# Optimization experiments

Measured on AMD Instinct MI355X. Metric: run time of the kernel, lower is better.

The kernel has to match this reference:

```python
import jax, jax.numpy as jnp
import numpy as np

H = 1024
N_HEADS = 8
HEAD_DIM = H // N_HEADS
META_DIM = 256
VOCAB = 32000
MIN_W, MAX_W = 0.1, 5.0
LN_EPS = 1e-5


def _ln(x, g, b):
    mu = jnp.mean(x, axis=-1, keepdims=True)
    var = jnp.var(x, axis=-1, keepdims=True)
    return (x - mu) * jax.lax.rsqrt(var + LN_EPS) * g + b


def setup_inputs() -> dict:
    key = jax.random.key(0)
    ks = jax.random.split(key, 16)
    B, S = 4, 2048
    s = 0.02
    return {
        "hidden_states": jax.random.normal(ks[0], (B, S, H), jnp.float32),
        "token_ids": jax.random.randint(ks[1], (B, S), 0, VOCAB, jnp.int32),
        "attention_mask": jnp.ones((B, S), jnp.bool_),
        "pos_embed": jax.random.normal(ks[2], (1, S, H), jnp.float32),
        # torch nn.MultiheadAttention params
        "in_proj_w": jax.random.normal(ks[3], (3 * H, H), jnp.float32) * s,
        "in_proj_b": jnp.zeros((3 * H,), jnp.float32),
        "out_w": jax.random.normal(ks[4], (H, H), jnp.float32) * s,
        "out_b": jnp.zeros((H,), jnp.float32),
        # meta_network params (torch Linear convention: y = x @ W.T + b)
        "w1": jax.random.normal(ks[5], (META_DIM, 2 * H), jnp.float32) * s,
        "b1": jnp.zeros((META_DIM,), jnp.float32),
        "g1": jnp.ones((META_DIM,), jnp.float32),
        "beta1": jnp.zeros((META_DIM,), jnp.float32),
        "w2": jax.random.normal(ks[6], (META_DIM // 2, META_DIM), jnp.float32) * s,
        "b2": jnp.zeros((META_DIM // 2,), jnp.float32),
        "g2": jnp.ones((META_DIM // 2,), jnp.float32),
        "beta2": jnp.zeros((META_DIM // 2,), jnp.float32),
        "w3": jax.random.normal(ks[7], (1, META_DIM // 2), jnp.float32) * s,
        "b3": jnp.zeros((1,), jnp.float32),
        # tensorized ImportanceMemory.get_importance: one scalar per vocab id
        "importance_table": jax.random.uniform(ks[8], (VOCAB,), jnp.float32) * 0.1,
    }


def reference(hidden_states, token_ids, attention_mask, pos_embed,
              in_proj_w, in_proj_b, out_w, out_b,
              w1, b1, g1, beta1, w2, b2, g2, beta2, w3, b3,
              importance_table):
    B, S, _ = hidden_states.shape
    x = hidden_states + pos_embed[:, :S, :]

    # MultiheadAttention (batch_first, eval mode -> no dropout)
    qkv = x @ in_proj_w.T + in_proj_b                      # [B,S,3H]
    q, k, v = jnp.split(qkv, 3, axis=-1)
    q = q.reshape(B, S, N_HEADS, HEAD_DIM)
    k = k.reshape(B, S, N_HEADS, HEAD_DIM)
    v = v.reshape(B, S, N_HEADS, HEAD_DIM)
    scores = jnp.einsum('bqhd,bkhd->bhqk', q, k) / jnp.sqrt(jnp.float32(HEAD_DIM))
    scores = jnp.where(attention_mask[:, None, None, :], scores, jnp.float32(-1e9))
    attn = jax.nn.softmax(scores, axis=-1)
    ctx = jnp.einsum('bhqk,bkhd->bqhd', attn, v).reshape(B, S, H)
    attended = ctx @ out_w.T + out_b

    combined = jnp.concatenate([x, attended], axis=-1)     # [B,S,2H]
    h = jax.nn.relu(_ln(combined @ w1.T + b1, g1, beta1))
    h = jax.nn.relu(_ln(h @ w2.T + b2, g2, beta2))
    base_weights = (h @ w3.T + b3).squeeze(-1)             # [B,S]

    # tensorized per-token importance lookup + clamp (manual_weights empty)
    importance = importance_table[token_ids]               # gather [B,S]
    weight = jnp.clip(base_weights * (1.0 + importance), MIN_W, MAX_W)
    return jnp.where(attention_mask, weight, 0.0)
```

## Files before the change

kernel.cpp:

```cpp
#include <hip/hip_runtime.h>
#include <hip/hip_bf16.h>
#include <math.h>

typedef __bf16 bf16;
typedef bf16 bf16x8 __attribute__((ext_vector_type(8)));
typedef bf16 bf16x4 __attribute__((ext_vector_type(4)));
typedef float f32x4 __attribute__((ext_vector_type(4)));

#define HDIM 1024
#define NHEADS 8
#define HD 128
#define MD1 256
#define MD2 128
#define LNEPS 1e-5f

__device__ __forceinline__ f32x4 mfma16(bf16x8 a, bf16x8 b, f32x4 c) {
  return __builtin_amdgcn_mfma_f32_16x16x32_bf16(a, b, c, 0, 0, 0);
}

__device__ __forceinline__ void gload_lds16(const bf16* g, bf16* l) {
  __builtin_amdgcn_global_load_lds(
      (const __attribute__((address_space(1))) void*)g,
      (__attribute__((address_space(3))) void*)l, 16, 0, 0);
}

__global__ void k_prep_all(
    const float* __restrict__ hs, const float* __restrict__ pos,
    bf16* __restrict__ xbf, int SH, int nprep,
    const float* __restrict__ s0, bf16* __restrict__ d0, int n0,
    const float* __restrict__ s1, bf16* __restrict__ d1, int n1,
    const float* __restrict__ s2, bf16* __restrict__ d2, int n2,
    const float* __restrict__ s3, bf16* __restrict__ d3, int n3) {
  int i = (blockIdx.x * blockDim.x + threadIdx.x) * 4;
  if (i < nprep) {
    float4 a = *(const float4*)(hs + i);
    float4 p = *(const float4*)(pos + (i % SH));
    bf16x4 o;
    o[0] = (bf16)(a.x + p.x); o[1] = (bf16)(a.y + p.y);
    o[2] = (bf16)(a.z + p.z); o[3] = (bf16)(a.w + p.w);
    *(bf16x4*)(xbf + i) = o;
    return;
  }
  int j = i - nprep;
  const float* s; bf16* d;
  if (j < n0)                { s = s0 + j; d = d0 + j; }
  else if (j < n0 + n1)      { s = s1 + (j - n0); d = d1 + (j - n0); }
  else if (j < n0 + n1 + n2) { s = s2 + (j - n0 - n1); d = d2 + (j - n0 - n1); }
  else                       { s = s3 + (j - n0 - n1 - n2); d = d3 + (j - n0 - n1 - n2); }
  float4 v = *(const float4*)s;
  bf16x4 o;
  o[0] = (bf16)v.x; o[1] = (bf16)v.y; o[2] = (bf16)v.z; o[3] = (bf16)v.w;
  *(bf16x4*)d = o;
}

template<bool OUT_BF>
__global__ __launch_bounds__(256) void k_gemm128(
    const bf16* __restrict__ A, const bf16* __restrict__ Bw,
    const float* __restrict__ bias, void* __restrict__ out,
    int N, int K) {
  __shared__ bf16 As[128 * 32];
  __shared__ bf16 Bs[128 * 32];
  const int tid = threadIdx.x;
  const int w = tid >> 6, lane = tid & 63;
  const int quad = lane >> 4, l16 = lane & 15;
  const int wm = w & 1, wn = w >> 1;
  const int tm = blockIdx.x * 128, tn = blockIdx.y * 128;

  const int r0 = tid >> 2;
  const int f0 = (r0 ^ (r0 >> 2)) & 3;
  const int f1 = ((r0 + 64) ^ ((r0 + 64) >> 2)) & 3;
  const int c0 = (((tid & 3) ^ f0) * 8);
  const int c1 = (((tid & 3) ^ f1) * 8);
  const bf16* a0 = A + (size_t)(tm + r0) * K + c0;
  const bf16* a1 = A + (size_t)(tm + r0 + 64) * K + c1;
  const bf16* b0 = Bw + (size_t)(tn + r0) * K + c0;
  const bf16* b1 = Bw + (size_t)(tn + r0 + 64) * K + c1;
  bf16* lA = As + (size_t)tid * 8;
  bf16* lB = Bs + (size_t)tid * 8;

  f32x4 acc[4][4] = {};
  for (int k0 = 0; k0 < K; k0 += 32) {
    gload_lds16(a0 + k0, lA);
    gload_lds16(a1 + k0, lA + 2048);
    gload_lds16(b0 + k0, lB);
    gload_lds16(b1 + k0, lB + 2048);
    __syncthreads();
    bf16x8 af[4], bfr[4];
#pragma unroll
    for (int mt = 0; mt < 4; ++mt) {
      const int r = wm * 64 + mt * 16 + l16;
      af[mt] = *(const bf16x8*)&As[r * 32 + ((quad ^ ((r ^ (r >> 2)) & 3)) << 3)];
    }
#pragma unroll
    for (int nt = 0; nt < 4; ++nt) {
      const int r = wn * 64 + nt * 16 + l16;
      bfr[nt] = *(const bf16x8*)&Bs[r * 32 + ((quad ^ ((r ^ (r >> 2)) & 3)) << 3)];
    }
#pragma unroll
    for (int mt = 0; mt < 4; ++mt)
#pragma unroll
      for (int nt = 0; nt < 4; ++nt)
        acc[mt][nt] = mfma16(af[mt], bfr[nt], acc[mt][nt]);
    __syncthreads();
  }

#pragma unroll
  for (int nt = 0; nt < 4; ++nt) {
    const int col = tn + wn * 64 + nt * 16 + l16;
    const float bv = bias ? bias[col] : 0.f;
#pragma unroll
    for (int mt = 0; mt < 4; ++mt) {
#pragma unroll
      for (int i = 0; i < 4; ++i) {
        const int row = tm + wm * 64 + mt * 16 + quad * 4 + i;
        const float v = acc[mt][nt][i] + bv;
        if (OUT_BF) ((bf16*)out)[(size_t)row * N + col] = (bf16)v;
        else        ((float*)out)[(size_t)row * N + col] = v;
      }
    }
  }
}

__global__ __launch_bounds__(256) void k_gemm_qkv(
    const bf16* __restrict__ A, const bf16* __restrict__ Bw,
    const float* __restrict__ bias, bf16* __restrict__ Qo,
    bf16* __restrict__ Ko, bf16* __restrict__ VTo, int S, int K) {
  __shared__ bf16 As[128 * 32];
  __shared__ bf16 Bs[128 * 32];
  const int tid = threadIdx.x;
  const int w = tid >> 6, lane = tid & 63;
  const int quad = lane >> 4, l16 = lane & 15;
  const int wm = w & 1, wn = w >> 1;
  const int tm = blockIdx.x * 128, tn = blockIdx.y * 128;

  const int r0 = tid >> 2;
  const int f0 = (r0 ^ (r0 >> 2)) & 3;
  const int f1 = ((r0 + 64) ^ ((r0 + 64) >> 2)) & 3;
  const int c0 = (((tid & 3) ^ f0) * 8);
  const int c1 = (((tid & 3) ^ f1) * 8);
  const bf16* a0 = A + (size_t)(tm + r0) * K + c0;
  const bf16* a1 = A + (size_t)(tm + r0 + 64) * K + c1;
  const bf16* b0 = Bw + (size_t)(tn + r0) * K + c0;
  const bf16* b1 = Bw + (size_t)(tn + r0 + 64) * K + c1;
  bf16* lA = As + (size_t)tid * 8;
  bf16* lB = Bs + (size_t)tid * 8;

  f32x4 acc[4][4] = {};
  for (int k0 = 0; k0 < K; k0 += 32) {
    gload_lds16(a0 + k0, lA);
    gload_lds16(a1 + k0, lA + 2048);
    gload_lds16(b0 + k0, lB);
    gload_lds16(b1 + k0, lB + 2048);
    __syncthreads();
    bf16x8 af[4], bfr[4];
#pragma unroll
    for (int mt = 0; mt < 4; ++mt) {
      const int r = wm * 64 + mt * 16 + l16;
      af[mt] = *(const bf16x8*)&As[r * 32 + ((quad ^ ((r ^ (r >> 2)) & 3)) << 3)];
    }
#pragma unroll
    for (int nt = 0; nt < 4; ++nt) {
      const int r = wn * 64 + nt * 16 + l16;
      bfr[nt] = *(const bf16x8*)&Bs[r * 32 + ((quad ^ ((r ^ (r >> 2)) & 3)) << 3)];
    }
#pragma unroll
    for (int mt = 0; mt < 4; ++mt)
#pragma unroll
      for (int nt = 0; nt < 4; ++nt)
        acc[mt][nt] = mfma16(af[mt], bfr[nt], acc[mt][nt]);
    __syncthreads();
  }

  const int region = tn >> 10;
  const int btile = tm / S, s0 = tm % S;
#pragma unroll
  for (int nt = 0; nt < 4; ++nt) {
    const int col = tn + wn * 64 + nt * 16 + l16;
    const float bv = bias[col];
#pragma unroll
    for (int mt = 0; mt < 4; ++mt) {
      if (region == 2) {
        const int d = col - 2048, hh = d >> 7, dd = d & 127;
        const int sb = s0 + wm * 64 + mt * 16 + quad * 4;
        bf16x4 o4;
#pragma unroll
        for (int i = 0; i < 4; ++i) o4[i] = (bf16)(acc[mt][nt][i] + bv);
        *(bf16x4*)&VTo[((size_t)(btile * NHEADS + hh) * HD + dd) * S + sb] = o4;
      } else {
        bf16* dst = (region == 0) ? Qo : Ko;
        const int cc = (region == 0) ? col : col - 1024;
#pragma unroll
        for (int i = 0; i < 4; ++i) {
          const int row = tm + wm * 64 + mt * 16 + quad * 4 + i;
          dst[(size_t)row * HDIM + cc] = (bf16)(acc[mt][nt][i] + bv);
        }
      }
    }
  }
}

__global__ __launch_bounds__(256) void k_flash(
    const bf16* __restrict__ Qg, const bf16* __restrict__ Kg,
    const bf16* __restrict__ VTg, const int* __restrict__ mask,
    bf16* __restrict__ ctx, int S) {
  __shared__ bf16 Ks[64][136];
  __shared__ bf16 Vt[128 * 64];
  __shared__ bf16 Ps[8 * 1024];
  __shared__ float biass[64];
  const int tid = threadIdx.x, w = tid >> 6, lane = tid & 63;
  const int quad = lane >> 4, l16 = lane & 15;
  const int bh = blockIdx.y, b = bh / NHEADS, h = bh % NHEADS;
  const int q0 = blockIdx.x * 128 + w * 32;
  const size_t bS = (size_t)b * S;
  const bf16* Qb = Qg + bS * HDIM + h * HD;
  const bf16* Kb = Kg + bS * HDIM + h * HD;
  const bf16* Vb = VTg + (size_t)bh * HD * S;
  const int* mrow = mask + bS;

  bf16x8 qf[2][4];
#pragma unroll
  for (int qt = 0; qt < 2; ++qt)
#pragma unroll
    for (int s = 0; s < 4; ++s)
      qf[qt][s] = *(const bf16x8*)(Qb + (size_t)(q0 + qt * 16 + l16) * HDIM + s * 32 + quad * 8);

  float lsum[2][4] = {};
  f32x4 o[2][8] = {};
  const float scale2 = 0.08838834764831845f * 1.4426950408889634f;

  const int nchunk = S / 64;
  bf16x8 kreg[4], vreg[4];
  int mreg = (tid < 64) ? mrow[tid] : 0;
#pragma unroll
  for (int it = 0; it < 4; ++it) {
    const int cid = tid + it * 256;
    kreg[it] = *(const bf16x8*)(Kb + (size_t)(cid >> 4) * HDIM + (cid & 15) * 8);
    vreg[it] = *(const bf16x8*)(Vb + (size_t)(cid >> 3) * S + (cid & 7) * 8);
  }

  for (int c0 = 0; c0 < nchunk; ++c0) {
    __syncthreads();
#pragma unroll
    for (int it = 0; it < 4; ++it) {
      const int cid = tid + it * 256;
      *(bf16x8*)&Ks[cid >> 4][(cid & 15) * 8] = kreg[it];
      const int vd = cid >> 3, vkb = cid & 7;
      *(bf16x8*)&Vt[vd * 64 + ((vkb ^ (vd & 7)) << 3)] = vreg[it];
    }
    if (tid < 64) biass[tid] = mreg ? 0.f : -1e9f;
    __syncthreads();
    const int key0n = ((c0 + 1 < nchunk) ? c0 + 1 : c0) * 64;
    if (tid < 64) mreg = mrow[key0n + tid];
#pragma unroll
    for (int it = 0; it < 4; ++it) {
      const int cid = tid + it * 256;
      kreg[it] = *(const bf16x8*)(Kb + (size_t)(key0n + (cid >> 4)) * HDIM + (cid & 15) * 8);
      vreg[it] = *(const bf16x8*)(Vb + (size_t)(cid >> 3) * S + key0n + (cid & 7) * 8);
    }
    f32x4 s4[2][4] = {};
#pragma unroll
    for (int g = 0; g < 4; ++g)
#pragma unroll
      for (int s = 0; s < 4; ++s) {
        bf16x8 kf = *(const bf16x8*)&Ks[g * 16 + l16][s * 32 + quad * 8];
        s4[0][g] = mfma16(qf[0][s], kf, s4[0][g]);
        s4[1][g] = mfma16(qf[1][s], kf, s4[1][g]);
      }
#pragma unroll
    for (int qt = 0; qt < 2; ++qt) {
      const int base = (w * 2 + qt) * 1024;
#pragma unroll
      for (int g = 0; g < 4; ++g) {
        const float bias = biass[g * 16 + l16];
        const int kb2 = 2 * g + (l16 >> 3), klo = l16 & 7;
#pragma unroll
        for (int i = 0; i < 4; ++i) {
          const float p = exp2f(fmaf(s4[qt][g][i], scale2, bias));
          lsum[qt][i] += p;
          const int r = quad * 4 + i, fr = (r ^ (r >> 3)) & 7;
          Ps[base + r * 64 + ((kb2 ^ fr) << 3) + klo] = (bf16)p;
        }
      }
    }
    const int fl = (l16 ^ (l16 >> 3)) & 7;
#pragma unroll
    for (int hh = 0; hh < 2; ++hh) {
      const int kb = hh * 4 + quad;
      bf16x8 pf0 = *(const bf16x8*)&Ps[(w * 2) * 1024 + l16 * 64 + ((kb ^ fl) << 3)];
      bf16x8 pf1 = *(const bf16x8*)&Ps[(w * 2 + 1) * 1024 + l16 * 64 + ((kb ^ fl) << 3)];
#pragma unroll
      for (int dg = 0; dg < 8; ++dg) {
        const int d = dg * 16 + l16;
        bf16x8 vf = *(const bf16x8*)&Vt[d * 64 + ((kb ^ (d & 7)) << 3)];
        o[0][dg] = mfma16(pf0, vf, o[0][dg]);
        o[1][dg] = mfma16(pf1, vf, o[1][dg]);
      }
    }
  }

#pragma unroll
  for (int qt = 0; qt < 2; ++qt)
#pragma unroll
    for (int i = 0; i < 4; ++i) {
      float ls = lsum[qt][i];
#pragma unroll
      for (int off = 1; off < 16; off <<= 1) ls += __shfl_xor(ls, off);
      const int row = q0 + qt * 16 + quad * 4 + i;
      const float inv = 1.0f / ls;
#pragma unroll
      for (int dg = 0; dg < 8; ++dg)
        ctx[(bS + row) * HDIM + h * HD + dg * 16 + l16] = (bf16)(o[qt][dg][i] * inv);
    }
}

__global__ __launch_bounds__(256) void k_meta1(
    const bf16* __restrict__ A1, const bf16* __restrict__ A2,
    const bf16* __restrict__ Bw, const float* __restrict__ b1,
    const float* __restrict__ g1, const float* __restrict__ be1,
    bf16* __restrict__ h1) {
  __shared__ bf16 As[64][40];
  __shared__ bf16 Bs[256][40];
  __shared__ float part_s[64][4];
  __shared__ float part_q[64][4];
  const int tid = threadIdx.x;
  const int w = tid >> 6, lane = tid & 63;
  const int quad = lane >> 4, l16 = lane & 15;
  const int tm = blockIdx.x * 64;
  const int lr = tid >> 2, lc = (tid & 3) * 8;

  f32x4 acc[4][4] = {};
  for (int k0 = 0; k0 < 2048; k0 += 32) {
    const int kg = k0 + lc;
    const bf16* ap = (kg < 1024) ? (A1 + (size_t)(tm + lr) * 1024 + kg)
                                 : (A2 + (size_t)(tm + lr) * 1024 + (kg - 1024));
    *(bf16x8*)&As[lr][lc] = *(const bf16x8*)ap;
#pragma unroll
    for (int it = 0; it < 4; ++it)
      *(bf16x8*)&Bs[lr + it * 64][lc] =
          *(const bf16x8*)(Bw + (size_t)(lr + it * 64) * 2048 + kg);
    __syncthreads();
    bf16x8 af[4], bfr[4];
#pragma unroll
    for (int mt = 0; mt < 4; ++mt) af[mt] = *(const bf16x8*)&As[mt * 16 + l16][quad * 8];
#pragma unroll
    for (int nt = 0; nt < 4; ++nt)
      bfr[nt] = *(const bf16x8*)&Bs[w * 64 + nt * 16 + l16][quad * 8];
#pragma unroll
    for (int mt = 0; mt < 4; ++mt)
#pragma unroll
      for (int nt = 0; nt < 4; ++nt)
        acc[mt][nt] = mfma16(af[mt], bfr[nt], acc[mt][nt]);
    __syncthreads();
  }

  float bv[4], gv[4], bev[4];
#pragma unroll
  for (int nt = 0; nt < 4; ++nt) {
    const int col = w * 64 + nt * 16 + l16;
    bv[nt] = b1[col]; gv[nt] = g1[col]; bev[nt] = be1[col];
  }
#pragma unroll
  for (int mt = 0; mt < 4; ++mt)
#pragma unroll
    for (int i = 0; i < 4; ++i) {
      float s = 0.f, q = 0.f;
#pragma unroll
      for (int nt = 0; nt < 4; ++nt) {
        const float v = acc[mt][nt][i] + bv[nt];
        s += v; q += v * v;
      }
#pragma unroll
      for (int off = 1; off < 16; off <<= 1) { s += __shfl_xor(s, off); q += __shfl_xor(q, off); }
      if (l16 == 0) {
        const int row = mt * 16 + quad * 4 + i;
        part_s[row][w] = s; part_q[row][w] = q;
      }
    }
  __syncthreads();
#pragma unroll
  for (int mt = 0; mt < 4; ++mt)
#pragma unroll
    for (int i = 0; i < 4; ++i) {
      const int row = mt * 16 + quad * 4 + i;
      const float4 ps = *(const float4*)part_s[row];
      const float4 pq = *(const float4*)part_q[row];
      const float sum = ps.x + ps.y + ps.z + ps.w;
      const float sq = pq.x + pq.y + pq.z + pq.w;
      const float mean = sum / MD1;
      const float var = sq / MD1 - mean * mean;
      const float r = rsqrtf(var + LNEPS);
      bf16* orow = h1 + (size_t)(tm + row) * MD1;
#pragma unroll
      for (int nt = 0; nt < 4; ++nt) {
        const int col = w * 64 + nt * 16 + l16;
        const float v = acc[mt][nt][i] + bv[nt];
        const float t = (v - mean) * r * gv[nt] + bev[nt];
        orow[col] = (bf16)fmaxf(t, 0.f);
      }
    }
}

__global__ __launch_bounds__(256) void k_meta2(
    const bf16* __restrict__ A, const bf16* __restrict__ Bw,
    const float* __restrict__ b2, const float* __restrict__ g2,
    const float* __restrict__ be2, const float* __restrict__ w3,
    const float* __restrict__ b3, const int* __restrict__ tok,
    const int* __restrict__ msk, const float* __restrict__ imp,
    float* __restrict__ out) {
  __shared__ bf16 As[64][40];
  __shared__ bf16 Bs[128][40];
  const int tid = threadIdx.x;
  const int w = tid >> 6, lane = tid & 63;
  const int quad = lane >> 4, l16 = lane & 15;
  const int tm = blockIdx.x * 64;
  const int lr = tid >> 2, lc = (tid & 3) * 8;

  f32x4 acc[8] = {};
  for (int k0 = 0; k0 < MD1; k0 += 32) {
    const int kg = k0 + lc;
    *(bf16x8*)&As[lr][lc] = *(const bf16x8*)(A + (size_t)(tm + lr) * MD1 + kg);
    if (lr < 64) {
#pragma unroll
      for (int it = 0; it < 2; ++it)
        *(bf16x8*)&Bs[lr + it * 64][lc] =
            *(const bf16x8*)(Bw + (size_t)(lr + it * 64) * MD1 + kg);
    }
    __syncthreads();
    bf16x8 af = *(const bf16x8*)&As[w * 16 + l16][quad * 8];
#pragma unroll
    for (int nt = 0; nt < 8; ++nt) {
      bf16x8 bfr = *(const bf16x8*)&Bs[nt * 16 + l16][quad * 8];
      acc[nt] = mfma16(af, bfr, acc[nt]);
    }
    __syncthreads();
  }

  float bv[8], gv[8], bev[8], w3v[8];
#pragma unroll
  for (int nt = 0; nt < 8; ++nt) {
    const int col = nt * 16 + l16;
    bv[nt] = b2[col]; gv[nt] = g2[col]; bev[nt] = be2[col]; w3v[nt] = w3[col];
  }
  const float b3v = b3[0];
#pragma unroll
  for (int i = 0; i < 4; ++i) {
    float s = 0.f, q = 0.f;
#pragma unroll
    for (int nt = 0; nt < 8; ++nt) {
      const float v = acc[nt][i] + bv[nt];
      s += v; q += v * v;
    }
#pragma unroll
    for (int off = 1; off < 16; off <<= 1) { s += __shfl_xor(s, off); q += __shfl_xor(q, off); }
    const float mean = s / MD2;
    const float var = q / MD2 - mean * mean;
    const float r = rsqrtf(var + LNEPS);
    float d = 0.f;
#pragma unroll
    for (int nt = 0; nt < 8; ++nt) {
      const float v = acc[nt][i] + bv[nt];
      const float t = (v - mean) * r * gv[nt] + bev[nt];
      d += fmaxf(t, 0.f) * w3v[nt];
    }
#pragma unroll
    for (int off = 1; off < 16; off <<= 1) d += __shfl_xor(d, off);
    if (l16 == 0) {
      const int row = tm + w * 16 + quad * 4 + i;
      const float base = d + b3v;
      float wt = base * (1.f + imp[tok[row]]);
      wt = fminf(fmaxf(wt, 0.1f), 5.0f);
      out[row] = msk[row] ? wt : 0.f;
    }
  }
}

extern "C" void kernel_launch(void* const* d_in, const int* in_sizes, int n_in,
                              void* d_out, int out_size, void* d_ws, size_t ws_size,
                              hipStream_t stream) {
  const float* hs  = (const float*)d_in[0];
  const int*   tok = (const int*)d_in[1];
  const int*   msk = (const int*)d_in[2];
  const float* pos = (const float*)d_in[3];
  const float* inw = (const float*)d_in[4];
  const float* inb = (const float*)d_in[5];
  const float* ow  = (const float*)d_in[6];
  const float* ob  = (const float*)d_in[7];
  const float* w1  = (const float*)d_in[8];
  const float* b1  = (const float*)d_in[9];
  const float* g1  = (const float*)d_in[10];
  const float* be1 = (const float*)d_in[11];
  const float* w2  = (const float*)d_in[12];
  const float* b2  = (const float*)d_in[13];
  const float* g2  = (const float*)d_in[14];
  const float* be2 = (const float*)d_in[15];
  const float* w3  = (const float*)d_in[16];
  const float* b3  = (const float*)d_in[17];
  const float* imp = (const float*)d_in[18];

  const int SH = in_sizes[3];
  const int S  = SH / HDIM;
  const int Bsz = in_sizes[0] / SH;
  const int M = Bsz * S;

  char* ws = (char*)d_ws;
  const size_t MB2 = (size_t)M * HDIM * 2;
  size_t off = 0;
  bf16* xbf = (bf16*)(ws + off);  off += MB2;
  bf16* Qb  = (bf16*)(ws + off);  off += MB2;
  bf16* Kb  = (bf16*)(ws + off);  off += MB2;
  bf16* VTb = (bf16*)(ws + off);  off += MB2;
  bf16* ctx = (bf16*)(ws + off);  off += MB2;
  bf16* winp = (bf16*)(ws + off); off += (size_t)3 * HDIM * HDIM * 2;
  bf16* wout = (bf16*)(ws + off); off += (size_t)HDIM * HDIM * 2;
  bf16* w1b = (bf16*)(ws + off);  off += (size_t)MD1 * 2 * HDIM * 2;
  bf16* w2b = (bf16*)(ws + off);  off += (size_t)MD2 * MD1 * 2;
  bf16* attbf = Qb;
  bf16* h1 = VTb;

  const int nprep = M * HDIM;
  const int n0 = 3 * HDIM * HDIM, n1 = HDIM * HDIM, n2 = MD1 * 2 * HDIM, n3 = MD2 * MD1;
  k_prep_all<<<(nprep + n0 + n1 + n2 + n3) / 4 / 256, 256, 0, stream>>>(
      hs, pos, xbf, SH, nprep, inw, winp, n0, ow, wout, n1, w1, w1b, n2, w2, w2b, n3);
  k_gemm_qkv<<<dim3(M / 128, (3 * HDIM) / 128), 256, 0, stream>>>(
      xbf, winp, inb, Qb, Kb, VTb, S, HDIM);
  k_flash<<<dim3(S / 128, Bsz * NHEADS), 256, 0, stream>>>(Qb, Kb, VTb, msk, ctx, S);
  k_gemm128<true><<<dim3(M / 128, HDIM / 128), 256, 0, stream>>>(
      ctx, wout, ob, attbf, HDIM, HDIM);
  k_meta1<<<M / 64, 256, 0, stream>>>(xbf, attbf, w1b, b1, g1, be1, h1);
  k_meta2<<<M / 64, 256, 0, stream>>>(h1, w2b, b2, g2, be2, w3, b3, tok, msk, imp,
                                      (float*)d_out);
}
```

Measured before the change: 429.1 us.

## Split flash attention over two key halves and fuse the meta MLP kernels

The flash attention kernel now splits the key range into two halves across a third grid dimension. Each half writes unnormalized bf16 partial outputs plus row sums, and a new combine kernel adds the halves and normalizes them. This doubles the block count to improve CU occupancy and latency hiding, at the cost of extra partial-output traffic, one more launch, and some bf16 rounding of unnormalized values. Separately, the two meta-network kernels are fused so the first layer's activations stay in shared memory instead of round-tripping through global memory.

```diff
diff --git a/kernel.cpp b/kernel.cpp
--- a/kernel.cpp
+++ b/kernel.cpp
@@ -202,7 +202,7 @@
 __global__ __launch_bounds__(256) void k_flash(
     const bf16* __restrict__ Qg, const bf16* __restrict__ Kg,
     const bf16* __restrict__ VTg, const int* __restrict__ mask,
-    bf16* __restrict__ ctx, int S) {
+    bf16* __restrict__ opart, float* __restrict__ lpart, int S, int Mtot) {
   __shared__ bf16 Ks[64][136];
   __shared__ bf16 Vt[128 * 64];
   __shared__ bf16 Ps[8 * 1024];
@@ -210,12 +210,16 @@
   const int tid = threadIdx.x, w = tid >> 6, lane = tid & 63;
   const int quad = lane >> 4, l16 = lane & 15;
   const int bh = blockIdx.y, b = bh / NHEADS, h = bh % NHEADS;
+  const int split = blockIdx.z;
+  const int klo = split * (S >> 1), khi = klo + (S >> 1);
   const int q0 = blockIdx.x * 128 + w * 32;
   const size_t bS = (size_t)b * S;
   const bf16* Qb = Qg + bS * HDIM + h * HD;
   const bf16* Kb = Kg + bS * HDIM + h * HD;
   const bf16* Vb = VTg + (size_t)bh * HD * S;
   const int* mrow = mask + bS;
+  bf16* op = opart + (size_t)split * Mtot * HDIM;
+  float* lp = lpart + (size_t)split * Mtot * NHEADS;
 
   bf16x8 qf[2][4];
 #pragma unroll
@@ -228,17 +232,16 @@
   f32x4 o[2][8] = {};
   const float scale2 = 0.08838834764831845f * 1.4426950408889634f;
 
-  const int nchunk = S / 64;
   bf16x8 kreg[4], vreg[4];
-  int mreg = (tid < 64) ? mrow[tid] : 0;
+  int mreg = (tid < 64) ? mrow[klo + tid] : 0;
 #pragma unroll
   for (int it = 0; it < 4; ++it) {
     const int cid = tid + it * 256;
-    kreg[it] = *(const bf16x8*)(Kb + (size_t)(cid >> 4) * HDIM + (cid & 15) * 8);
-    vreg[it] = *(const bf16x8*)(Vb + (size_t)(cid >> 3) * S + (cid & 7) * 8);
-  }
-
-  for (int c0 = 0; c0 < nchunk; ++c0) {
+    kreg[it] = *(const bf16x8*)(Kb + (size_t)(klo + (cid >> 4)) * HDIM + (cid & 15) * 8);
+    vreg[it] = *(const bf16x8*)(Vb + (size_t)(cid >> 3) * S + klo + (cid & 7) * 8);
+  }
+
+  for (int key0 = klo; key0 < khi; key0 += 64) {
     __syncthreads();
 #pragma unroll
     for (int it = 0; it < 4; ++it) {
@@ -249,7 +252,7 @@
     }
     if (tid < 64) biass[tid] = mreg ? 0.f : -1e9f;
     __syncthreads();
-    const int key0n = ((c0 + 1 < nchunk) ? c0 + 1 : c0) * 64;
+    const int key0n = (key0 + 64 < khi) ? key0 + 64 : key0;
     if (tid < 64) mreg = mrow[key0n + tid];
 #pragma unroll
     for (int it = 0; it < 4; ++it) {
@@ -272,13 +275,13 @@
 #pragma unroll
       for (int g = 0; g < 4; ++g) {
         const float bias = biass[g * 16 + l16];
-        const int kb2 = 2 * g + (l16 >> 3), klo = l16 & 7;
+        const int kb2 = 2 * g + (l16 >> 3), klo2 = l16 & 7;
 #pragma unroll
         for (int i = 0; i < 4; ++i) {
           const float p = exp2f(fmaf(s4[qt][g][i], scale2, bias));
           lsum[qt][i] += p;
           const int r = quad * 4 + i, fr = (r ^ (r >> 3)) & 7;
-          Ps[base + r * 64 + ((kb2 ^ fr) << 3) + klo] = (bf16)p;
+          Ps[base + r * 64 + ((kb2 ^ fr) << 3) + klo2] = (bf16)p;
         }
       }
     }
@@ -306,22 +309,45 @@
 #pragma unroll
       for (int off = 1; off < 16; off <<= 1) ls += __shfl_xor(ls, off);
       const int row = q0 + qt * 16 + quad * 4 + i;
-      const float inv = 1.0f / ls;
+      if (l16 == 0) lp[(bS + row) * NHEADS + h] = ls;
 #pragma unroll
       for (int dg = 0; dg < 8; ++dg)
-        ctx[(bS + row) * HDIM + h * HD + dg * 16 + l16] = (bf16)(o[qt][dg][i] * inv);
-    }
-}
-
-__global__ __launch_bounds__(256) void k_meta1(
+        op[(bS + row) * HDIM + h * HD + dg * 16 + l16] = (bf16)o[qt][dg][i];
+    }
+}
+
+__global__ void k_combine(bf16* __restrict__ op0, const bf16* __restrict__ op1,
+                          const float* __restrict__ lpart, int Mtot) {
+  const int idx = (blockIdx.x * blockDim.x + threadIdx.x) * 4;
+  const int row = idx >> 10;
+  const int h = (idx & 1023) >> 7;
+  const float l = lpart[row * NHEADS + h] +
+                  lpart[(size_t)Mtot * NHEADS + row * NHEADS + h];
+  const float inv = 1.0f / l;
+  bf16x4 a = *(const bf16x4*)&op0[idx];
+  bf16x4 b = *(const bf16x4*)&op1[idx];
+  bf16x4 o;
+#pragma unroll
+  for (int j = 0; j < 4; ++j) o[j] = (bf16)(((float)a[j] + (float)b[j]) * inv);
+  *(bf16x4*)&op0[idx] = o;
+}
+
+__global__ __launch_bounds__(256) void k_meta12(
     const bf16* __restrict__ A1, const bf16* __restrict__ A2,
-    const bf16* __restrict__ Bw, const float* __restrict__ b1,
+    const bf16* __restrict__ Bw1, const float* __restrict__ b1,
     const float* __restrict__ g1, const float* __restrict__ be1,
-    bf16* __restrict__ h1) {
-  __shared__ bf16 As[64][40];
-  __shared__ bf16 Bs[256][40];
+    const bf16* __restrict__ Bw2, const float* __restrict__ b2,
+    const float* __restrict__ g2, const float* __restrict__ be2,
+    const float* __restrict__ w3, const float* __restrict__ b3,
+    const int* __restrict__ tok, const int* __restrict__ msk,
+    const float* __restrict__ imp, float* __restrict__ out) {
+  __shared__ char smem[44032];
   __shared__ float part_s[64][4];
   __shared__ float part_q[64][4];
+  bf16 (*As)[40]  = (bf16(*)[40])smem;
+  bf16 (*Bs)[40]  = (bf16(*)[40])(smem + 5120);
+  bf16 (*h1s)[264] = (bf16(*)[264])smem;
+  bf16 (*Bs2)[40] = (bf16(*)[40])(smem + 33792);
   const int tid = threadIdx.x;
   const int w = tid >> 6, lane = tid & 63;
   const int quad = lane >> 4, l16 = lane & 15;
@@ -337,7 +363,7 @@
 #pragma unroll
     for (int it = 0; it < 4; ++it)
       *(bf16x8*)&Bs[lr + it * 64][lc] =
-          *(const bf16x8*)(Bw + (size_t)(lr + it * 64) * 2048 + kg);
+          *(const bf16x8*)(Bw1 + (size_t)(lr + it * 64) * 2048 + kg);
     __syncthreads();
     bf16x8 af[4], bfr[4];
 #pragma unroll
@@ -389,57 +415,38 @@
       const float mean = sum / MD1;
       const float var = sq / MD1 - mean * mean;
       const float r = rsqrtf(var + LNEPS);
-      bf16* orow = h1 + (size_t)(tm + row) * MD1;
 #pragma unroll
       for (int nt = 0; nt < 4; ++nt) {
         const int col = w * 64 + nt * 16 + l16;
         const float v = acc[mt][nt][i] + bv[nt];
         const float t = (v - mean) * r * gv[nt] + bev[nt];
-        orow[col] = (bf16)fmaxf(t, 0.f);
-      }
-    }
-}
-
-__global__ __launch_bounds__(256) void k_meta2(
-    const bf16* __restrict__ A, const bf16* __restrict__ Bw,
-    const float* __restrict__ b2, const float* __restrict__ g2,
-    const float* __restrict__ be2, const float* __restrict__ w3,
-    const float* __restrict__ b3, const int* __restrict__ tok,
-    const int* __restrict__ msk, const float* __restrict__ imp,
-    float* __restrict__ out) {
-  __shared__ bf16 As[64][40];
-  __shared__ bf16 Bs[128][40];
-  const int tid = threadIdx.x;
-  const int w = tid >> 6, lane = tid & 63;
-  const int quad = lane >> 4, l16 = lane & 15;
-  const int tm = blockIdx.x * 64;
-  const int lr = tid >> 2, lc = (tid & 3) * 8;
-
-  f32x4 acc[8] = {};
+        h1s[row][col] = (bf16)fmaxf(t, 0.f);
+      }
+    }
+  __syncthreads();
+
+  f32x4 acc2[8] = {};
   for (int k0 = 0; k0 < MD1; k0 += 32) {
     const int kg = k0 + lc;
-    *(bf16x8*)&As[lr][lc] = *(const bf16x8*)(A + (size_t)(tm + lr) * MD1 + kg);
-    if (lr < 64) {
-#pragma unroll
-      for (int it = 0; it < 2; ++it)
-        *(bf16x8*)&Bs[lr + it * 64][lc] =
-            *(const bf16x8*)(Bw + (size_t)(lr + it * 64) * MD1 + kg);
-    }
-    __syncthreads();
-    bf16x8 af = *(const bf16x8*)&As[w * 16 + l16][quad * 8];
+#pragma unroll
+    for (int it = 0; it < 2; ++it)
+      *(bf16x8*)&Bs2[lr + it * 64][lc] =
+          *(const bf16x8*)(Bw2 + (size_t)(lr + it * 64) * MD1 + kg);
+    __syncthreads();
+    bf16x8 af = *(const bf16x8*)&h1s[w * 16 + l16][k0 + quad * 8];
 #pragma unroll
     for (int nt = 0; nt < 8; ++nt) {
-      bf16x8 bfr = *(const bf16x8*)&Bs[nt * 16 + l16][quad * 8];
-      acc[nt] = mfma16(af, bfr, acc[nt]);
-    }
-    __syncthreads();
-  }
-
-  float bv[8], gv[8], bev[8], w3v[8];
+      bf16x8 bfr = *(const bf16x8*)&Bs2[nt * 16 + l16][quad * 8];
+      acc2[nt] = mfma16(af, bfr, acc2[nt]);
+    }
+    __syncthreads();
+  }
+
+  float bv2[8], gv2[8], bev2[8], w3v[8];
 #pragma unroll
   for (int nt = 0; nt < 8; ++nt) {
     const int col = nt * 16 + l16;
-    bv[nt] = b2[col]; gv[nt] = g2[col]; bev[nt] = be2[col]; w3v[nt] = w3[col];
+    bv2[nt] = b2[col]; gv2[nt] = g2[col]; bev2[nt] = be2[col]; w3v[nt] = w3[col];
   }
   const float b3v = b3[0];
 #pragma unroll
@@ -447,7 +454,7 @@
     float s = 0.f, q = 0.f;
 #pragma unroll
     for (int nt = 0; nt < 8; ++nt) {
-      const float v = acc[nt][i] + bv[nt];
+      const float v = acc2[nt][i] + bv2[nt];
       s += v; q += v * v;
     }
 #pragma unroll
@@ -458,8 +465,8 @@
     float d = 0.f;
 #pragma unroll
     for (int nt = 0; nt < 8; ++nt) {
-      const float v = acc[nt][i] + bv[nt];
-      const float t = (v - mean) * r * gv[nt] + bev[nt];
+      const float v = acc2[nt][i] + bv2[nt];
+      const float t = (v - mean) * r * gv2[nt] + bev2[nt];
       d += fmaxf(t, 0.f) * w3v[nt];
     }
 #pragma unroll
@@ -509,13 +516,14 @@
   bf16* Qb  = (bf16*)(ws + off);  off += MB2;
   bf16* Kb  = (bf16*)(ws + off);  off += MB2;
   bf16* VTb = (bf16*)(ws + off);  off += MB2;
-  bf16* ctx = (bf16*)(ws + off);  off += MB2;
+  bf16* op0 = (bf16*)(ws + off);  off += MB2;
+  bf16* op1 = (bf16*)(ws + off);  off += MB2;
   bf16* winp = (bf16*)(ws + off); off += (size_t)3 * HDIM * HDIM * 2;
   bf16* wout = (bf16*)(ws + off); off += (size_t)HDIM * HDIM * 2;
   bf16* w1b = (bf16*)(ws + off);  off += (size_t)MD1 * 2 * HDIM * 2;
   bf16* w2b = (bf16*)(ws + off);  off += (size_t)MD2 * MD1 * 2;
+  float* lpart = (float*)(ws + off); off += (size_t)2 * M * NHEADS * 4;
   bf16* attbf = Qb;
-  bf16* h1 = VTb;
 
   const int nprep = M * HDIM;
   const int n0 = 3 * HDIM * HDIM, n1 = HDIM * HDIM, n2 = MD1 * 2 * HDIM, n3 = MD2 * MD1;
@@ -523,10 +531,12 @@
       hs, pos, xbf, SH, nprep, inw, winp, n0, ow, wout, n1, w1, w1b, n2, w2, w2b, n3);
   k_gemm_qkv<<<dim3(M / 128, (3 * HDIM) / 128), 256, 0, stream>>>(
       xbf, winp, inb, Qb, Kb, VTb, S, HDIM);
-  k_flash<<<dim3(S / 128, Bsz * NHEADS), 256, 0, stream>>>(Qb, Kb, VTb, msk, ctx, S);
+  k_flash<<<dim3(S / 128, Bsz * NHEADS, 2), 256, 0, stream>>>(
+      Qb, Kb, VTb, msk, op0, lpart, S, M);
+  k_combine<<<(M * HDIM / 4) / 256, 256, 0, stream>>>(op0, op1, lpart, M);
   k_gemm128<true><<<dim3(M / 128, HDIM / 128), 256, 0, stream>>>(
-      ctx, wout, ob, attbf, HDIM, HDIM);
-  k_meta1<<<M / 64, 256, 0, stream>>>(xbf, attbf, w1b, b1, g1, be1, h1);
-  k_meta2<<<M / 64, 256, 0, stream>>>(h1, w2b, b2, g2, be2, w3, b3, tok, msk, imp,
-                                      (float*)d_out);
-}
+      op0, wout, ob, attbf, HDIM, HDIM);
+  k_meta12<<<M / 64, 256, 0, stream>>>(xbf, attbf, w1b, b1, g1, be1,
+                                       w2b, b2, g2, be2, w3, b3, tok, msk, imp,
+                                       (float*)d_out);
+}
```

After: 435.6 us. No clear change (+1.5%).
